# Optimization experiments

Measured on AMD Instinct MI355X. Metric: run time of the kernel, lower is better.

The kernel has to match this reference:

```python
import jax, jax.numpy as jnp
import numpy as np
from jax import lax

K = 4
H = 1024
IN = 512
OUT = 8192
T = 128
B = 32


def setup_inputs() -> dict:
    key = jax.random.key(0)
    ks = jax.random.split(key, 5)
    return {
        "X": jax.random.normal(ks[0], (T, B, IN), dtype=jnp.float32),
        "Wxh_w": jax.random.normal(ks[1], (H, IN), dtype=jnp.float32) * 0.02,
        "Wxh_b": jax.random.normal(ks[2], (H,), dtype=jnp.float32) * 0.02,
        "Whh_w": jax.random.normal(ks[3], (H, (K - 1) * H), dtype=jnp.float32) * 0.02,
        "Wmo_w": jax.random.normal(ks[4], (OUT, K * H), dtype=jnp.float32) * 0.02,
    }


def reference(X, Wxh_w, Wxh_b, Whh_w, Wmo_w):
    batch = X.shape[1]
    # history stack hs: [K-1, B, H], hs[0] = oldest, hs[-1] = newest
    hs0 = jnp.zeros((K - 1, batch, H), dtype=X.dtype)

    def step(hs, x_t):
        # concat reversed(h_prevs): newest block first -> [B, (K-1)*H]
        h_cat = hs[::-1].transpose(1, 0, 2).reshape(batch, (K - 1) * H)
        h_t = jax.nn.selu(x_t @ Wxh_w.T + Wxh_b + h_cat @ Whh_w.T)  # [B, H]
        h_out = jnp.concatenate([h_t, h_cat], axis=1)  # [B, K*H]
        out_t = h_out @ Wmo_w.T  # [B, OUT]
        new_hs = jnp.concatenate([hs[1:], h_t[None]], axis=0)
        # truncated BPTT: detach the (new) oldest hidden
        new_hs = new_hs.at[0].set(lax.stop_gradient(new_hs[0]))
        return new_hs, out_t

    _, outs = lax.scan(step, hs0, X)
    return outs  # [T, B, OUT]
```

## Files before the change

### kernel.cpp

```cpp
#include <hip/hip_runtime.h>
#include <hip/hip_bf16.h>

#define T_STEPS 128
#define BATCH   32
#define IN_DIM  512
#define H_DIM   1024
#define OUT_DIM 8192
#define KH      3072
#define NWG     128
#define SLOT_E  32768
#define NSLOT   131

typedef __attribute__((ext_vector_type(8))) short short8;
typedef __attribute__((ext_vector_type(4))) float f32x4;

__device__ __forceinline__ unsigned short bf16_rne(float f) {
  unsigned u = __float_as_uint(f);
  unsigned r = (u + 0x7FFFu + ((u >> 16) & 1u)) >> 16;
  return (unsigned short)r;
}

__device__ __forceinline__ void gload_lds16(const void* g, void* l) {
  __builtin_amdgcn_global_load_lds(
      (const __attribute__((address_space(1))) void*)g,
      (__attribute__((address_space(3))) void*)l, 16, 0, 0);
}

__global__ __launch_bounds__(256) void convert_kernel(
    const float* __restrict__ src, unsigned short* __restrict__ dst, int n4) {
  int i = blockIdx.x * blockDim.x + threadIdx.x;
  const int stride = gridDim.x * blockDim.x;
  for (; i < n4; i += stride) {
    float4 v = ((const float4*)src)[i];
    ushort4 o;
    o.x = bf16_rne(v.x); o.y = bf16_rne(v.y);
    o.z = bf16_rne(v.z); o.w = bf16_rne(v.w);
    ((ushort4*)dst)[i] = o;
  }
}

__global__ __launch_bounds__(256) void pre_kernel(
    const float* __restrict__ X, const float* __restrict__ Wxh,
    const float* __restrict__ bias, float* __restrict__ preT) {
  __shared__ float xs[32][260];
  const int tid = threadIdx.x;
  const int t  = blockIdx.x >> 4;
  const int jb = blockIdx.x & 15;
  const int b  = tid & 31;
  const int jg = tid >> 5;
  float acc[8];
  #pragma unroll
  for (int i = 0; i < 8; ++i) acc[i] = 0.f;

  for (int kc = 0; kc < 2; ++kc) {
    __syncthreads();
    #pragma unroll
    for (int v = tid; v < 2048; v += 256) {
      int br = v >> 6, i4 = v & 63;
      float4 x4 = *(const float4*)(X + (size_t)t*(BATCH*IN_DIM) + (size_t)br*IN_DIM + kc*256 + i4*4);
      *(float4*)&xs[br][i4*4] = x4;
    }
    __syncthreads();
    for (int i = 0; i < 256; i += 4) {
      const int k = kc*256 + i;
      float4 xv = *(const float4*)&xs[b][i];
      #pragma unroll
      for (int jj = 0; jj < 8; ++jj) {
        const int j = jb*64 + jg + jj*8;
        float4 w4 = *(const float4*)(Wxh + (size_t)j*IN_DIM + k);
        acc[jj] += xv.x*w4.x + xv.y*w4.y + xv.z*w4.z + xv.w*w4.w;
      }
    }
  }
  #pragma unroll
  for (int jj = 0; jj < 8; ++jj) {
    const int j = jb*64 + jg + jj*8;
    preT[(size_t)t*(H_DIM*BATCH) + (size_t)j*BATCH + b] = acc[jj] + bias[jj*8 ? j : j];
  }
}

template<int RN, int RD1, int RD2>
__device__ __forceinline__ void do_step(
    const int t, const int tid, const int wg, const int j0,
    const int lane, const int wv,
    const short8* __restrict__ wf, const short8* __restrict__ hi8,
    const short8* __restrict__ lo8, const float* __restrict__ preT,
    unsigned short* __restrict__ hHi, unsigned short* __restrict__ hLo,
    int* __restrict__ grp, int* __restrict__ root,
    short8 (&Rh0)[3][4], short8 (&Rh1)[3][4],
    short8 (&Rl0)[3][4], short8 (&Rl1)[3][4],
    float (&red)[8][16][33],
    unsigned short (&hpk_hi)[32][8], unsigned short (&hpk_lo)[32][8]) {
  f32x4 a0h = {}, a0l = {}, a1h = {}, a1l = {};

  #pragma unroll
  for (int i = 0; i < 4; ++i) {
    const int ks = 32 + wv*4 + i;
    const short8 af = wf[ks*64 + lane];
    a0h = __builtin_amdgcn_mfma_f32_16x16x32_bf16(af, Rh0[RD1][i], a0h, 0, 0, 0);
    a1h = __builtin_amdgcn_mfma_f32_16x16x32_bf16(af, Rh1[RD1][i], a1h, 0, 0, 0);
    a0l = __builtin_amdgcn_mfma_f32_16x16x32_bf16(af, Rl0[RD1][i], a0l, 0, 0, 0);
    a1l = __builtin_amdgcn_mfma_f32_16x16x32_bf16(af, Rl1[RD1][i], a1l, 0, 0, 0);
  }
  #pragma unroll
  for (int i = 0; i < 4; ++i) {
    const int ks = 64 + wv*4 + i;
    const short8 af = wf[ks*64 + lane];
    a0h = __builtin_amdgcn_mfma_f32_16x16x32_bf16(af, Rh0[RD2][i], a0h, 0, 0, 0);
    a1h = __builtin_amdgcn_mfma_f32_16x16x32_bf16(af, Rh1[RD2][i], a1h, 0, 0, 0);
    a0l = __builtin_amdgcn_mfma_f32_16x16x32_bf16(af, Rl0[RD2][i], a0l, 0, 0, 0);
    a1l = __builtin_amdgcn_mfma_f32_16x16x32_bf16(af, Rl1[RD2][i], a1l, 0, 0, 0);
  }

  float upre = 0.f;
  if (tid < 256)
    upre = preT[(size_t)t*(H_DIM*BATCH) + (size_t)(j0 + (tid >> 5))*BATCH + (tid & 31)];

  if (t > 0) {
    if (tid == 0) {
      while (__hip_atomic_load(&root[(t-1) << 4], __ATOMIC_RELAXED, __HIP_MEMORY_SCOPE_AGENT) < 16)
        __builtin_amdgcn_s_sleep(1);
    }
    __syncthreads();
    asm volatile("" ::: "memory");
  }

  {
    const size_t sb = (size_t)(128 - t) * 4096;
    #pragma unroll
    for (int i = 0; i < 4; ++i) {
      const int ks = wv*4 + i;
      const size_t bidx = sb + (size_t)ks*128 + (size_t)(lane >> 4)*32 + (lane & 15);
      Rh0[RN][i] = hi8[bidx];
      Rh1[RN][i] = hi8[bidx + 16];
      Rl0[RN][i] = lo8[bidx];
      Rl1[RN][i] = lo8[bidx + 16];
    }
  }
  #pragma unroll
  for (int i = 0; i < 4; ++i) {
    const int ks = wv*4 + i;
    const short8 af = wf[ks*64 + lane];
    a0h = __builtin_amdgcn_mfma_f32_16x16x32_bf16(af, Rh0[RN][i], a0h, 0, 0, 0);
    a1h = __builtin_amdgcn_mfma_f32_16x16x32_bf16(af, Rh1[RN][i], a1h, 0, 0, 0);
    a0l = __builtin_amdgcn_mfma_f32_16x16x32_bf16(af, Rl0[RN][i], a0l, 0, 0, 0);
    a1l = __builtin_amdgcn_mfma_f32_16x16x32_bf16(af, Rl1[RN][i], a1l, 0, 0, 0);
  }

  const f32x4 s0 = a0h + a0l;
  const f32x4 s1 = a1h + a1l;
  const int rr = (lane >> 4) * 4, cc = lane & 15;
  #pragma unroll
  for (int q = 0; q < 4; ++q) {
    red[wv][rr + q][cc]      = s0[q];
    red[wv][rr + q][16 + cc] = s1[q];
  }
  __syncthreads();

  if (tid < 256) {
    const int jj = tid >> 5, b = tid & 31;
    float u = upre;
    #pragma unroll
    for (int w = 0; w < 8; ++w)
      u += red[w][jj][b] + red[w][jj + 8][b];
    const float h = u > 0.f ? 1.0507009873554805f*u
                            : (1.0507009873554805f*1.6732632423543772f)*expm1f(u);
    const unsigned short hh = bf16_rne(h);
    hpk_hi[b][jj] = hh;
    hpk_lo[b][jj] = bf16_rne(h - __uint_as_float((unsigned)hh << 16));
  }
  __syncthreads();

  if (tid < 32) {
    const int b = tid;
    const size_t base = (size_t)(127 - t)*SLOT_E + (size_t)(j0 >> 3)*256 + (size_t)b*8;
    const unsigned long long h0 = *(const unsigned long long*)&hpk_hi[b][0];
    const unsigned long long h1 = *(const unsigned long long*)&hpk_hi[b][4];
    const unsigned long long l0 = *(const unsigned long long*)&hpk_lo[b][0];
    const unsigned long long l1 = *(const unsigned long long*)&hpk_lo[b][4];
    __hip_atomic_store((unsigned long long*)(hHi + base),     h0, __ATOMIC_RELAXED, __HIP_MEMORY_SCOPE_AGENT);
    __hip_atomic_store((unsigned long long*)(hHi + base) + 1, h1, __ATOMIC_RELAXED, __HIP_MEMORY_SCOPE_AGENT);
    __hip_atomic_store((unsigned long long*)(hLo + base),     l0, __ATOMIC_RELAXED, __HIP_MEMORY_SCOPE_AGENT);
    __hip_atomic_store((unsigned long long*)(hLo + base) + 1, l1, __ATOMIC_RELAXED, __HIP_MEMORY_SCOPE_AGENT);
    asm volatile("s_waitcnt vmcnt(0)" ::: "memory");
    if (tid == 0) {
      const int g = wg >> 3;
      if (__hip_atomic_fetch_add(&grp[((t << 4) + g) << 4], 1, __ATOMIC_RELAXED, __HIP_MEMORY_SCOPE_AGENT) == 7)
        __hip_atomic_fetch_add(&root[t << 4], 1, __ATOMIC_RELAXED, __HIP_MEMORY_SCOPE_AGENT);
    }
  }
}

__global__ __launch_bounds__(512, 2) void recur_kernel(
    const float* __restrict__ Whh, const float* __restrict__ preT,
    unsigned short* __restrict__ hHi, unsigned short* __restrict__ hLo,
    int* __restrict__ grp, int* __restrict__ root) {
  __shared__ __align__(16) unsigned short w_lds[96*64*8];
  __shared__ float red[8][16][33];
  __shared__ __align__(16) unsigned short hpk_hi[32][8];
  __shared__ __align__(16) unsigned short hpk_lo[32][8];
  const int tid  = threadIdx.x;
  const int wg   = blockIdx.x;
  const int j0   = wg * 8;
  const int lane = tid & 63;
  const int wv   = tid >> 6;

  for (int s = tid; s < 6144; s += 512) {
    const int ks = s >> 6, l = s & 63;
    const int r = l & 15;
    const int j = j0 + (r & 7);
    const int part = r >> 3;
    const int kb = ks*32 + (l >> 4)*8;
    const float* wp = Whh + (size_t)j*KH + kb;
    unsigned short tmp[8];
    #pragma unroll
    for (int i = 0; i < 8; ++i) {
      const float f = wp[i];
      unsigned short v = bf16_rne(f);
      if (part) v = bf16_rne(f - __uint_as_float((unsigned)v << 16));
      tmp[i] = v;
    }
    *(short8*)&w_lds[s*8] = *(short8*)tmp;
  }
  __syncthreads();

  const short8* wf  = (const short8*)w_lds;
  const short8* hi8 = (const short8*)hHi;
  const short8* lo8 = (const short8*)hLo;

  short8 Rh0[3][4], Rh1[3][4], Rl0[3][4], Rl1[3][4];
  const short8 z8 = {};
  #pragma unroll
  for (int r = 1; r < 3; ++r)
    #pragma unroll
    for (int i = 0; i < 4; ++i) {
      Rh0[r][i] = z8; Rh1[r][i] = z8; Rl0[r][i] = z8; Rl1[r][i] = z8;
    }

  for (int t3 = 0; t3 < 126; t3 += 3) {
    do_step<0,2,1>(t3,   tid, wg, j0, lane, wv, wf, hi8, lo8, preT, hHi, hLo,
                   grp, root, Rh0, Rh1, Rl0, Rl1, red, hpk_hi, hpk_lo);
    do_step<1,0,2>(t3+1, tid, wg, j0, lane, wv, wf, hi8, lo8, preT, hHi, hLo,
                   grp, root, Rh0, Rh1, Rl0, Rl1, red, hpk_hi, hpk_lo);
    do_step<2,1,0>(t3+2, tid, wg, j0, lane, wv, wf, hi8, lo8, preT, hHi, hLo,
                   grp, root, Rh0, Rh1, Rl0, Rl1, red, hpk_hi, hpk_lo);
  }
  do_step<0,2,1>(126, tid, wg, j0, lane, wv, wf, hi8, lo8, preT, hHi, hLo,
                 grp, root, Rh0, Rh1, Rl0, Rl1, red, hpk_hi, hpk_lo);
  do_step<1,0,2>(127, tid, wg, j0, lane, wv, wf, hi8, lo8, preT, hHi, hLo,
                 grp, root, Rh0, Rh1, Rl0, Rl1, red, hpk_hi, hpk_lo);
}

__global__ __launch_bounds__(256) void gemm_kernel(
    const unsigned short* __restrict__ Ah, const unsigned short* __restrict__ Bm,
    float* __restrict__ C) {
  __shared__ __align__(16) unsigned short lA[4096];
  __shared__ __align__(16) unsigned short lB[4096];
  const int tid = threadIdx.x;
  const int wg = blockIdx.x;
  const int x = wg & 7;
  const int c = wg >> 3;
  const int mb = (x >> 2)*16 + (c & 15);
  const int nb = (x & 3)*16 + (c >> 4);
  const int lane = tid & 63;
  const int wv = tid >> 6;
  const int wm = wv >> 1, wn = wv & 1;
  const int lrow = lane & 15, lhalf = lane >> 4;
  const int rowB = tid >> 2, qB = tid & 3;
  f32x4 acc[4][4] = {};

  for (int kt = 0; kt < 128; ++kt) {
    __syncthreads();
    #pragma unroll
    for (int it = 0; it < 2; ++it) {
      const int idx = it*4 + wv;
      const int t  = mb*4 + (idx >> 1);
      gload_lds16(Ah + (size_t)(127 - t)*SLOT_E + kt*1024 + (idx & 1)*512 + (size_t)lane*8,
                  &lA[idx*512]);
      const int row = it*64 + rowB;
      gload_lds16(Bm + (size_t)(nb*128 + row)*4096 + kt*32 + qB*8,
                  &lB[(tid & 192)*8 + it*2048]);
    }
    __syncthreads();
    short8 af[4], bf[4];
    #pragma unroll
    for (int mi = 0; mi < 4; ++mi) {
      const int tg = wm*2 + (mi >> 1);
      af[mi] = *(const short8*)&lA[tg*1024 + lhalf*256 + (lrow + (mi & 1)*16)*8];
    }
    #pragma unroll
    for (int ni = 0; ni < 4; ++ni)
      bf[ni] = *(const short8*)&lB[(wn*64 + ni*16 + lrow)*32 + lhalf*8];
    #pragma unroll
    for (int mi = 0; mi < 4; ++mi)
      #pragma unroll
      for (int ni = 0; ni < 4; ++ni)
        acc[mi][ni] = __builtin_amdgcn_mfma_f32_16x16x32_bf16(af[mi], bf[ni], acc[mi][ni], 0, 0, 0);
  }
  const int orow0 = mb*128 + wm*64 + lhalf*4;
  const int ocol0 = nb*128 + wn*64 + lrow;
  #pragma unroll
  for (int mi = 0; mi < 4; ++mi)
    #pragma unroll
    for (int ni = 0; ni < 4; ++ni)
      #pragma unroll
      for (int q = 0; q < 4; ++q)
        __builtin_nontemporal_store(acc[mi][ni][q],
            &C[(size_t)(orow0 + mi*16 + q)*OUT_DIM + ocol0 + ni*16]);
}

extern "C" void kernel_launch(void* const* d_in, const int* in_sizes, int n_in,
                              void* d_out, int out_size, void* d_ws, size_t ws_size,
                              hipStream_t stream) {
  (void)in_sizes; (void)n_in; (void)out_size; (void)ws_size;
  const float* X   = (const float*)d_in[0];
  const float* Wxh = (const float*)d_in[1];
  const float* Wxb = (const float*)d_in[2];
  const float* Whh = (const float*)d_in[3];
  const float* Wmo = (const float*)d_in[4];
  float* out = (float*)d_out;
  char* ws = (char*)d_ws;

  const size_t OFF_PRET = 0;
  const size_t OFF_HHI  = OFF_PRET + (size_t)T_STEPS*H_DIM*BATCH*4;
  const size_t OFF_HLO  = OFF_HHI + (size_t)NSLOT*SLOT_E*2;
  const size_t OFF_GRP  = OFF_HLO + (size_t)NSLOT*SLOT_E*2;
  const size_t OFF_ROOT = OFF_GRP + (size_t)T_STEPS*16*64;
  const size_t OFF_W16  = OFF_ROOT + (size_t)T_STEPS*64;

  float* preT = (float*)(ws + OFF_PRET);
  unsigned short* hHi = (unsigned short*)(ws + OFF_HHI);
  unsigned short* hLo = (unsigned short*)(ws + OFF_HLO);
  int* grp  = (int*)(ws + OFF_GRP);
  int* root = (int*)(ws + OFF_ROOT);
  unsigned short* Wmo16 = (unsigned short*)(ws + OFF_W16);

  hipMemsetAsync(hHi + (size_t)128*SLOT_E, 0, (size_t)3*SLOT_E*2, stream);
  hipMemsetAsync(hLo + (size_t)128*SLOT_E, 0, (size_t)3*SLOT_E*2, stream);
  hipMemsetAsync(grp, 0, (size_t)T_STEPS*16*64 + (size_t)T_STEPS*64, stream);

  convert_kernel<<<2048, 256, 0, stream>>>(Wmo, Wmo16, (int)((size_t)OUT_DIM*4096/4));
  pre_kernel<<<2048, 256, 0, stream>>>(X, Wxh, Wxb, preT);
  recur_kernel<<<NWG, 512, 0, stream>>>(Whh, preT, hHi, hLo, grp, root);
  gemm_kernel<<<2048, 256, 0, stream>>>(hHi, Wmo16, out);
}
```

Before: 1.209 ms.

## Double-buffer LDS in output GEMM and swizzle B tile to avoid bank conflicts

The output GEMM kernel now uses two LDS buffers, so the global-to-LDS loads for the next K tile are issued before the MFMAs on the current tile, with explicit vmcnt waits. The B tile's 16-byte chunks are XOR-swizzled by row when stored and read, to reduce LDS bank conflicts on the fragment reads. A redundant bias index expression is also simplified. LDS use doubles and correctness depends on the vmcnt count matching the number of outstanding loads.

```diff
diff --git a/kernel.cpp b/kernel.cpp
--- a/kernel.cpp
+++ b/kernel.cpp
@@ -75,7 +75,7 @@
   #pragma unroll
   for (int jj = 0; jj < 8; ++jj) {
     const int j = jb*64 + jg + jj*8;
-    preT[(size_t)t*(H_DIM*BATCH) + (size_t)j*BATCH + b] = acc[jj] + bias[jj*8 ? j : j];
+    preT[(size_t)t*(H_DIM*BATCH) + (size_t)j*BATCH + b] = acc[jj] + bias[j];
   }
 }
 
@@ -254,8 +254,8 @@
 __global__ __launch_bounds__(256) void gemm_kernel(
     const unsigned short* __restrict__ Ah, const unsigned short* __restrict__ Bm,
     float* __restrict__ C) {
-  __shared__ __align__(16) unsigned short lA[4096];
-  __shared__ __align__(16) unsigned short lB[4096];
+  __shared__ __align__(16) unsigned short lA[2][4096];
+  __shared__ __align__(16) unsigned short lB[2][4096];
   const int tid = threadIdx.x;
   const int wg = blockIdx.x;
   const int x = wg & 7;
@@ -266,37 +266,54 @@
   const int wv = tid >> 6;
   const int wm = wv >> 1, wn = wv & 1;
   const int lrow = lane & 15, lhalf = lane >> 4;
-  const int rowB = tid >> 2, qB = tid & 3;
+  const int rowB0 = tid >> 2, qB = tid & 3;
   f32x4 acc[4][4] = {};
 
+#define STAGE(buf, kt) do {                                                    \
+    _Pragma("unroll")                                                          \
+    for (int it = 0; it < 2; ++it) {                                           \
+      const int idxA = it*4 + wv;                                              \
+      const int tA = mb*4 + (idxA >> 1);                                       \
+      gload_lds16(Ah + (size_t)(127 - tA)*SLOT_E + (size_t)(kt)*1024           \
+                     + (idxA & 1)*512 + (size_t)lane*8,                        \
+                  &lA[buf][idxA*512]);                                         \
+      const int rB = it*64 + rowB0;                                            \
+      const int qs = qB ^ ((rB ^ (rB >> 2)) & 3);                              \
+      gload_lds16(Bm + (size_t)(nb*128 + rB)*4096 + (size_t)(kt)*32 + qs*8,    \
+                  &lB[buf][(tid & 192)*8 + it*2048]);                          \
+    } } while (0)
+
+  STAGE(0, 0);
   for (int kt = 0; kt < 128; ++kt) {
-    __syncthreads();
-    #pragma unroll
-    for (int it = 0; it < 2; ++it) {
-      const int idx = it*4 + wv;
-      const int t  = mb*4 + (idx >> 1);
-      gload_lds16(Ah + (size_t)(127 - t)*SLOT_E + kt*1024 + (idx & 1)*512 + (size_t)lane*8,
-                  &lA[idx*512]);
-      const int row = it*64 + rowB;
-      gload_lds16(Bm + (size_t)(nb*128 + row)*4096 + kt*32 + qB*8,
-                  &lB[(tid & 192)*8 + it*2048]);
+    const int cur = kt & 1;
+    if (kt < 127) {
+      STAGE(cur ^ 1, kt + 1);
+      asm volatile("s_waitcnt vmcnt(4)" ::: "memory");
+    } else {
+      asm volatile("s_waitcnt vmcnt(0)" ::: "memory");
     }
     __syncthreads();
     short8 af[4], bf[4];
     #pragma unroll
     for (int mi = 0; mi < 4; ++mi) {
       const int tg = wm*2 + (mi >> 1);
-      af[mi] = *(const short8*)&lA[tg*1024 + lhalf*256 + (lrow + (mi & 1)*16)*8];
-    }
-    #pragma unroll
-    for (int ni = 0; ni < 4; ++ni)
-      bf[ni] = *(const short8*)&lB[(wn*64 + ni*16 + lrow)*32 + lhalf*8];
+      af[mi] = *(const short8*)&lA[cur][tg*1024 + lhalf*256 + (lrow + (mi & 1)*16)*8];
+    }
+    #pragma unroll
+    for (int ni = 0; ni < 4; ++ni) {
+      const int r = wn*64 + ni*16 + lrow;
+      const int qs = lhalf ^ ((r ^ (r >> 2)) & 3);
+      bf[ni] = *(const short8*)&lB[cur][r*32 + qs*8];
+    }
     #pragma unroll
     for (int mi = 0; mi < 4; ++mi)
       #pragma unroll
       for (int ni = 0; ni < 4; ++ni)
         acc[mi][ni] = __builtin_amdgcn_mfma_f32_16x16x32_bf16(af[mi], bf[ni], acc[mi][ni], 0, 0, 0);
-  }
+    __syncthreads();
+  }
+#undef STAGE
+
   const int orow0 = mb*128 + wm*64 + lhalf*4;
   const int ocol0 = nb*128 + wn*64 + lrow;
   #pragma unroll
```

Result: faster. 1.163 ms (-3.8%).
